# Kernel optimization log

Hardware: AMD Instinct MI355X
Metric: run time of the kernel (lower is better)

Reference implementation:

```python
import jax, jax.numpy as jnp
import numpy as np
import math

H = 16
D_MODEL = 1024
D_K = D_MODEL // H
B, S = 4, 2048
NEG = -1.0e9


def setup_inputs() -> dict:
    key = jax.random.key(0)
    ks = jax.random.split(key, 13)
    scale = 1.0 / math.sqrt(D_MODEL)
    inp = {
        "query": jax.random.normal(ks[0], (B, S, D_MODEL), jnp.float32),
        "key": jax.random.normal(ks[1], (B, S, D_MODEL), jnp.float32),
        "value": jax.random.normal(ks[2], (B, S, D_MODEL), jnp.float32),
        "mask": jax.random.randint(ks[3], (B, S), 0, 2, jnp.int32),
        "Wq": jax.random.normal(ks[4], (D_MODEL, D_MODEL), jnp.float32) * scale,
        "bq": jax.random.normal(ks[5], (D_MODEL,), jnp.float32) * scale,
        "Wk": jax.random.normal(ks[6], (D_MODEL, D_MODEL), jnp.float32) * scale,
        "bk": jax.random.normal(ks[7], (D_MODEL,), jnp.float32) * scale,
        "Wv": jax.random.normal(ks[8], (D_MODEL, D_MODEL), jnp.float32) * scale,
        "bv": jax.random.normal(ks[9], (D_MODEL,), jnp.float32) * scale,
        "Wo": jax.random.normal(ks[10], (D_MODEL, D_MODEL), jnp.float32) * scale,
        "bo": jax.random.normal(ks[11], (D_MODEL,), jnp.float32) * scale,
    }
    return inp


def _split_heads(x):
    # [B, S, D] -> [B, H, S, D_K]
    b, s, _ = x.shape
    return x.reshape(b, s, H, D_K).transpose(0, 2, 1, 3)


def reference(query, key, value, mask, Wq, bq, Wk, bk, Wv, bv, Wo, bo):
    # torch nn.Linear: y = x @ W.T + b
    q = _split_heads(query @ Wq.T + bq)
    k = _split_heads(key @ Wk.T + bk)
    v = _split_heads(value @ Wv.T + bv)
    scores = jnp.einsum("bhqd,bhkd->bhqk", q, k) / math.sqrt(D_K)
    # [B, S] key-padding mask -> broadcast as [B, 1, 1, S] (== torch's [B,1,S,S] repeat)
    m = mask[:, None, None, :]
    scores = jnp.where(m == 0, NEG, scores)
    p = jax.nn.softmax(scores, axis=-1)
    out = jnp.einsum("bhqk,bhkd->bhqd", p, v)  # [B, H, S, D_K]
    out = out.transpose(0, 2, 1, 3).reshape(query.shape[0], -1, D_MODEL)
    return out @ Wo.T + bo
```

## Files before the change

kernel.cpp:

```cpp
#include <hip/hip_runtime.h>


#define DMODEL 1024
#define SLEN 2048
#define NHEAD 16
#define LOG2E 1.44269504088896340736f

typedef __attribute__((ext_vector_type(4))) float f32x4;
typedef __attribute__((ext_vector_type(8))) short bf16x8;
typedef __attribute__((ext_vector_type(4))) int i32x4;
typedef __attribute__((ext_vector_type(2))) int i32x2;

__device__ __forceinline__ unsigned short f2bf(float f) {
  __bf16 h = (__bf16)f;
  union { __bf16 h; unsigned short u; } cv; cv.h = h; return cv.u;
}
__device__ __forceinline__ unsigned pk(float a, float b) {
  return (unsigned)f2bf(a) | ((unsigned)f2bf(b) << 16);
}
__device__ __forceinline__ float fexp2(float x) {
  float r;
  asm("v_exp_f32 %0, %1" : "=v"(r) : "v"(x));
  return r;
}
__device__ __forceinline__ f32x4 zero4() {
  f32x4 z; z[0] = 0.f; z[1] = 0.f; z[2] = 0.f; z[3] = 0.f; return z;
}
__device__ __forceinline__ void gload16(const void* g, void* l) {
  __builtin_amdgcn_global_load_lds(
      (const __attribute__((address_space(1))) unsigned int*)(uintptr_t)g,
      (__attribute__((address_space(3))) unsigned int*)(uintptr_t)l, 16, 0, 0);
}
__device__ __forceinline__ void barrier_lgkm() {
  asm volatile("s_waitcnt lgkmcnt(0)" ::: "memory");
  __builtin_amdgcn_s_barrier();
  __builtin_amdgcn_sched_barrier(0);
}

__global__ __launch_bounds__(256)
void gemm_qkv(const float* __restrict__ xq, const float* __restrict__ xk,
              const float* __restrict__ xv,
              const float* __restrict__ Wq, const float* __restrict__ bq,
              const float* __restrict__ Wk, const float* __restrict__ bk,
              const float* __restrict__ Wv, const float* __restrict__ bv,
              unsigned short* __restrict__ qw, unsigned short* __restrict__ kw,
              unsigned short* __restrict__ vw)
{
  const int bid = blockIdx.x;
  const int wg = (bid & 7) * 192 + (bid >> 3);
  const int z = wg >> 9;
  const int r = wg & 511;
  const int m0 = (r >> 3) * 128;
  const int n0 = (r & 7) * 128;

  const float* __restrict__ X    = (z == 0) ? xq : (z == 1) ? xk : xv;
  const float* __restrict__ W    = (z == 0) ? Wq : (z == 1) ? Wk : Wv;
  const float* __restrict__ bias = (z == 0) ? bq : (z == 1) ? bk : bv;
  const float scale = (z == 0) ? 0.125f * LOG2E : 1.0f;

  const int tid = threadIdx.x;
  const int lane = tid & 63, wid = tid >> 6;
  const int l15 = lane & 15, g = lane >> 4;
  const int wr = wid >> 1, wc = wid & 1;

  __shared__ __align__(16) char LDS[32768];
  unsigned short* TT = (unsigned short*)LDS;

  const int srow = tid >> 1, sh = tid & 1;
  const float* __restrict__ Ag = X + (size_t)(m0 + srow) * DMODEL + sh * 16;
  const float* __restrict__ Bg = W + (size_t)(n0 + srow) * DMODEL + sh * 16;
  const unsigned sw0 = (unsigned)(srow * 64) + (((unsigned)(sh * 2))     ^ ((unsigned)((srow >> 1) & 3))) * 16;
  const unsigned sw1 = (unsigned)(srow * 64) + (((unsigned)(sh * 2 + 1)) ^ ((unsigned)((srow >> 1) & 3))) * 16;

  f32x4 ar4[4], br4[4];
  auto loadA = [&](int kt2) {
    const float* p = Ag + kt2 * 32;
#pragma unroll
    for (int j = 0; j < 4; ++j) ar4[j] = *(const f32x4*)(p + j * 4);
  };
  auto loadB = [&](int kt2) {
    const float* p = Bg + kt2 * 32;
#pragma unroll
    for (int j = 0; j < 4; ++j) br4[j] = *(const f32x4*)(p + j * 4);
  };
  auto packA = [&](int bufsel) {
    char* Ab = LDS + bufsel * 8192;
    i32x4 wv0, wv1;
    wv0[0] = (int)pk(ar4[0][0], ar4[0][1]); wv0[1] = (int)pk(ar4[0][2], ar4[0][3]);
    wv0[2] = (int)pk(ar4[1][0], ar4[1][1]); wv0[3] = (int)pk(ar4[1][2], ar4[1][3]);
    wv1[0] = (int)pk(ar4[2][0], ar4[2][1]); wv1[1] = (int)pk(ar4[2][2], ar4[2][3]);
    wv1[2] = (int)pk(ar4[3][0], ar4[3][1]); wv1[3] = (int)pk(ar4[3][2], ar4[3][3]);
    *(i32x4*)(Ab + sw0) = wv0;
    *(i32x4*)(Ab + sw1) = wv1;
  };
  auto packB = [&](int bufsel) {
    char* Bb = LDS + 16384 + bufsel * 8192;
    i32x4 wv0, wv1;
    wv0[0] = (int)pk(br4[0][0], br4[0][1]); wv0[1] = (int)pk(br4[0][2], br4[0][3]);
    wv0[2] = (int)pk(br4[1][0], br4[1][1]); wv0[3] = (int)pk(br4[1][2], br4[1][3]);
    wv1[0] = (int)pk(br4[2][0], br4[2][1]); wv1[1] = (int)pk(br4[2][2], br4[2][3]);
    wv1[2] = (int)pk(br4[3][0], br4[3][1]); wv1[3] = (int)pk(br4[3][2], br4[3][3]);
    *(i32x4*)(Bb + sw0) = wv0;
    *(i32x4*)(Bb + sw1) = wv1;
  };

  f32x4 acc[4][4];
#pragma unroll
  for (int i = 0; i < 4; ++i)
#pragma unroll
    for (int j = 0; j < 4; ++j) acc[i][j] = zero4();

  loadA(0); loadB(0);
  packA(0); packB(0);
  loadA(1); loadB(1);
  __syncthreads();

  for (int kt = 0; kt < 32; ++kt) {
    const int cur = kt & 1;
    if (kt + 1 < 32) {
      packA(cur ^ 1);
      packB(cur ^ 1);
    }
    if (kt + 2 < 32) {
      loadA(kt + 2);
      loadB(kt + 2);
    }

    const char* Ab = LDS + cur * 8192;
    const char* Bb = LDS + 16384 + cur * 8192;
    bf16x8 afr[4], bfr[4];
#pragma unroll
    for (int i = 0; i < 4; ++i) {
      const int ra = wr * 64 + i * 16 + l15;
      afr[i] = *(const bf16x8*)(Ab + ra * 64 + ((g ^ ((ra >> 1) & 3)) * 16));
      const int rb = wc * 64 + i * 16 + l15;
      bfr[i] = *(const bf16x8*)(Bb + rb * 64 + ((g ^ ((rb >> 1) & 3)) * 16));
    }
#pragma unroll
    for (int mi = 0; mi < 4; ++mi)
#pragma unroll
      for (int ni = 0; ni < 4; ++ni)
        acc[mi][ni] = __builtin_amdgcn_mfma_f32_16x16x32_bf16(
            afr[mi], bfr[ni], acc[mi][ni], 0, 0, 0);

    if (kt + 1 < 32) barrier_lgkm();
  }

  float bv4[4];
#pragma unroll
  for (int ni = 0; ni < 4; ++ni) bv4[ni] = bias[n0 + wc * 64 + ni * 16 + l15];

  if (z == 2) {
    const int bb = m0 >> 11, s0 = m0 & 2047;
#pragma unroll
    for (int p = 0; p < 2; ++p) {
      __syncthreads();
      if (wc == p) {
#pragma unroll
        for (int mi = 0; mi < 4; ++mi)
#pragma unroll
          for (int ni = 0; ni < 4; ++ni)
#pragma unroll
            for (int rr2 = 0; rr2 < 4; ++rr2)
              TT[(ni * 16 + l15) * 136 + wr * 64 + mi * 16 + 4 * g + rr2] =
                  f2bf(acc[mi][ni][rr2] + bv4[ni]);
      }
      __syncthreads();
      const int rr = tid >> 2, cc = (tid & 3) * 32;
      unsigned short* dp = vw + ((size_t)(bb * 1024 + n0 + p * 64 + rr)) * 2048 + s0 + cc;
      const unsigned short* sp = &TT[rr * 136 + cc];
#pragma unroll
      for (int j = 0; j < 4; ++j)
        *(i32x4*)(void*)(dp + j * 8) = *(const i32x4*)(const void*)(sp + j * 8);
    }
    return;
  }

  unsigned short* __restrict__ dst = (z == 0) ? qw : kw;
#pragma unroll
  for (int mi = 0; mi < 4; ++mi) {
#pragma unroll
    for (int ni = 0; ni < 4; ++ni) {
      const int n = n0 + wc * 64 + ni * 16 + l15;
      const int h = n >> 6, d = n & 63;
#pragma unroll
      for (int rr2 = 0; rr2 < 4; ++rr2) {
        const int m = m0 + wr * 64 + mi * 16 + 4 * g + rr2;
        const int b = m >> 11, s = m & 2047;
        const float val = (acc[mi][ni][rr2] + bv4[ni]) * scale;
        dst[((size_t)(b * NHEAD + h) * SLEN + s) * 64 + d] = f2bf(val);
      }
    }
  }
}

__global__ __launch_bounds__(256, 3)
void attn(const unsigned short* __restrict__ q_ws,
          const unsigned short* __restrict__ k_ws,
          const unsigned short* __restrict__ vT,
              const int* __restrict__ mask,
          unsigned short* __restrict__ o_ws)
{
  const int bh = blockIdx.x;
  const int qt = blockIdx.y;
  const int b = bh >> 4, h = bh & 15;
  const int tid = threadIdx.x, w = tid >> 6, lane = tid & 63;
  const int l15 = lane & 15, g = lane >> 4;

  __shared__ __align__(16) unsigned short Kb[2][64 * 64];
  __shared__ __align__(16) unsigned short Vb[2][64 * 64];
  __shared__ __align__(16) unsigned short Pl[4][16 * 64];
  __shared__ __align__(16) float maskf[2048];

  {
    const int4* mp = (const int4*)(mask + b * SLEN);
    const int4 ma = mp[tid * 2], mb = mp[tid * 2 + 1];
    float4 f0, f1;
    f0.x = ma.x ? 0.f : -1e9f; f0.y = ma.y ? 0.f : -1e9f;
    f0.z = ma.z ? 0.f : -1e9f; f0.w = ma.w ? 0.f : -1e9f;
    f1.x = mb.x ? 0.f : -1e9f; f1.y = mb.y ? 0.f : -1e9f;
    f1.z = mb.z ? 0.f : -1e9f; f1.w = mb.w ? 0.f : -1e9f;
    *(float4*)&maskf[tid * 8]     = f0;
    *(float4*)&maskf[tid * 8 + 4] = f1;
  }

  const size_t head = (size_t)bh * SLEN;
  const int r8 = lane >> 3, c8 = lane & 7;
  const int swz = ((c8 ^ r8) * 16);
  const unsigned pswz = (unsigned)((l15 & 7) << 4);

  const int qbase = qt * 128 + w * 32;
  bf16x8 qf[2][2];
  {
    const unsigned short* qp0 = q_ws + (head + qbase + l15) * 64;
    const unsigned short* qp1 = q_ws + (head + qbase + 16 + l15) * 64;
    qf[0][0] = *(const bf16x8*)(qp0 + g * 8);
    qf[0][1] = *(const bf16x8*)(qp0 + 32 + g * 8);
    qf[1][0] = *(const bf16x8*)(qp1 + g * 8);
    qf[1][1] = *(const bf16x8*)(qp1 + 32 + g * 8);
  }

  auto stage = [&](int kt2, int bufi) {
#pragma unroll
    for (int cl = 0; cl < 2; ++cl) {
      const int rr = w * 16 + cl * 8 + r8;
      const char* gk = (const char*)(k_ws + (head + kt2 * 64 + rr) * 64) + swz;
      gload16(gk, &Kb[bufi][(w * 16 + cl * 8) * 64]);
      const char* gv = (const char*)(vT + ((size_t)(bh * 64 + rr)) * SLEN + kt2 * 64) + swz;
      gload16(gv, &Vb[bufi][(w * 16 + cl * 8) * 64]);
    }
  };

  stage(0, 0);
  __syncthreads();

  float m_run[2] = {-1e30f, -1e30f};
  float l_run[2] = {0.f, 0.f};
  f32x4 of[2][4];
#pragma unroll
  for (int qi = 0; qi < 2; ++qi)
#pragma unroll
    for (int n = 0; n < 4; ++n) of[qi][n] = zero4();

  unsigned short* Pw = (unsigned short*)Pl[w];
  int cur = 0;

  for (int kt = 0; kt < 32; ++kt) {
    if (kt + 1 < 32) stage(kt + 1, cur ^ 1);
    const char* Kc = (const char*)Kb[cur];
    const char* Vc = (const char*)Vb[cur];
    const int kv0 = kt * 64;

    f32x4 mv[4];
#pragma unroll
    for (int s = 0; s < 4; ++s) mv[s] = *(const f32x4*)&maskf[kv0 + s * 16 + g * 4];

#pragma unroll
    for (int qi = 0; qi < 2; ++qi) {
      f32x4 sac[4];
#pragma unroll
      for (int s = 0; s < 4; ++s) {
        const char* kr = Kc + (s * 16 + l15) * 128;
        const bf16x8 kf0 = *(const bf16x8*)(kr + ((unsigned)(g * 16) ^ pswz));
        const bf16x8 kf1 = *(const bf16x8*)(kr + ((unsigned)(64 + g * 16) ^ pswz));
        f32x4 zt = mv[s];
        zt = __builtin_amdgcn_mfma_f32_16x16x32_bf16(kf0, qf[qi][0], zt, 0, 0, 0);
        sac[s] = __builtin_amdgcn_mfma_f32_16x16x32_bf16(kf1, qf[qi][1], zt, 0, 0, 0);
      }

      float tmax = -3.0e38f;
#pragma unroll
      for (int s = 0; s < 4; ++s)
#pragma unroll
        for (int rr = 0; rr < 4; ++rr) tmax = fmaxf(tmax, sac[s][rr]);
      tmax = fmaxf(tmax, __shfl_xor(tmax, 16));
      tmax = fmaxf(tmax, __shfl_xor(tmax, 32));
      if (!__all(tmax <= m_run[qi] + 8.f)) {
        const float mnew = fmaxf(m_run[qi], tmax);
        const float alpha = fexp2(m_run[qi] - mnew);
        float af[4];
#pragma unroll
        for (int rr = 0; rr < 4; ++rr) af[rr] = __shfl(alpha, g * 4 + rr);
#pragma unroll
        for (int n = 0; n < 4; ++n)
#pragma unroll
          for (int rr = 0; rr < 4; ++rr) of[qi][n][rr] *= af[rr];
        l_run[qi] *= alpha;
        m_run[qi] = mnew;
      }
      float psum = 0.f;
      unsigned pr[4][2];
#pragma unroll
      for (int s = 0; s < 4; ++s) {
        const float p0 = fexp2(sac[s][0] - m_run[qi]);
        const float p1 = fexp2(sac[s][1] - m_run[qi]);
        const float p2 = fexp2(sac[s][2] - m_run[qi]);
        const float p3 = fexp2(sac[s][3] - m_run[qi]);
        psum += (p0 + p1) + (p2 + p3);
        pr[s][0] = pk(p0, p1); pr[s][1] = pk(p2, p3);
      }
      l_run[qi] += psum;
#pragma unroll
      for (int s = 0; s < 4; ++s) {
        i32x2 wv; wv[0] = (int)pr[s][0]; wv[1] = (int)pr[s][1];
        *(i32x2*)(void*)((char*)Pw + l15 * 128 + ((unsigned)(s * 32 + g * 8) ^ pswz)) = wv;
      }

#pragma unroll
      for (int k2 = 0; k2 < 2; ++k2) {
        const bf16x8 pa = *(const bf16x8*)(const void*)(
            (const char*)Pw + l15 * 128 + ((unsigned)(k2 * 64 + g * 16) ^ pswz));
#pragma unroll
        for (int n = 0; n < 4; ++n) {
          const bf16x8 vf = *(const bf16x8*)(
              Vc + (n * 16 + l15) * 128 + ((unsigned)(k2 * 64 + g * 16) ^ pswz));
          of[qi][n] = __builtin_amdgcn_mfma_f32_16x16x32_bf16(pa, vf, of[qi][n], 0, 0, 0);
        }
      }
    }
    __syncthreads();
    cur ^= 1;
  }

#pragma unroll
  for (int qi = 0; qi < 2; ++qi) {
    float lt = l_run[qi];
    lt += __shfl_xor(lt, 16);
    lt += __shfl_xor(lt, 32);
    float inv[4];
#pragma unroll
    for (int rr = 0; rr < 4; ++rr) inv[rr] = 1.f / __shfl(lt, g * 4 + rr);
    const int qrow0 = qt * 128 + w * 32 + qi * 16;
#pragma unroll
    for (int n = 0; n < 4; ++n) {
      const int d = h * 64 + n * 16 + l15;
#pragma unroll
      for (int rr = 0; rr < 4; ++rr) {
        const int sr = qrow0 + 4 * g + rr;
        o_ws[((size_t)b * SLEN + sr) * DMODEL + d] = f2bf(of[qi][n][rr] * inv[rr]);
      }
    }
  }
}

__global__ __launch_bounds__(256)
void gemm_out(const unsigned short* __restrict__ ow,
              const float* __restrict__ Wo, const float* __restrict__ bo,
              float* __restrict__ out)
{
  const int bid = blockIdx.x;
  const int wg = (bid & 7) * 64 + (bid >> 3);
  const int m0 = (wg >> 3) * 128;
  const int n0 = (wg & 7) * 128;

  const int tid = threadIdx.x;
  const int lane = tid & 63, wid = tid >> 6;
  const int l15 = lane & 15, g = lane >> 4;
  const int wr = wid >> 1, wc = wid & 1;

  __shared__ __align__(16) char LDS[32768];

  const int srow = tid >> 1, sh = tid & 1;
  const unsigned short* __restrict__ Ag = ow + (size_t)(m0 + srow) * DMODEL + sh * 16;
  const float* __restrict__ Bg = Wo + (size_t)(n0 + srow) * DMODEL + sh * 16;
  const unsigned sw0 = (unsigned)(srow * 64) + (((unsigned)(sh * 2))     ^ ((unsigned)((srow >> 1) & 3))) * 16;
  const unsigned sw1 = (unsigned)(srow * 64) + (((unsigned)(sh * 2 + 1)) ^ ((unsigned)((srow >> 1) & 3))) * 16;

  i32x4 ar2[2];
  f32x4 br4[4];
  auto loadA = [&](int kt2) {
    const unsigned short* p = Ag + kt2 * 32;
    ar2[0] = *(const i32x4*)(p);
    ar2[1] = *(const i32x4*)(p + 8);
  };
  auto loadB = [&](int kt2) {
    const float* p = Bg + kt2 * 32;
#pragma unroll
    for (int j = 0; j < 4; ++j) br4[j] = *(const f32x4*)(p + j * 4);
  };
  auto packA = [&](int bufsel) {
    char* Ab = LDS + bufsel * 8192;
    *(i32x4*)(Ab + sw0) = ar2[0];
    *(i32x4*)(Ab + sw1) = ar2[1];
  };
  auto packB = [&](int bufsel) {
    char* Bb = LDS + 16384 + bufsel * 8192;
    i32x4 wv0, wv1;
    wv0[0] = (int)pk(br4[0][0], br4[0][1]); wv0[1] = (int)pk(br4[0][2], br4[0][3]);
    wv0[2] = (int)pk(br4[1][0], br4[1][1]); wv0[3] = (int)pk(br4[1][2], br4[1][3]);
    wv1[0] = (int)pk(br4[2][0], br4[2][1]); wv1[1] = (int)pk(br4[2][2], br4[2][3]);
    wv1[2] = (int)pk(br4[3][0], br4[3][1]); wv1[3] = (int)pk(br4[3][2], br4[3][3]);
    *(i32x4*)(Bb + sw0) = wv0;
    *(i32x4*)(Bb + sw1) = wv1;
  };

  f32x4 acc[4][4];
#pragma unroll
  for (int i = 0; i < 4; ++i)
#pragma unroll
    for (int j = 0; j < 4; ++j) acc[i][j] = zero4();

  loadA(0); loadB(0);
  packA(0); packB(0);
  loadA(1); loadB(1);
  __syncthreads();

  for (int kt = 0; kt < 32; ++kt) {
    const int cur = kt & 1;
    if (kt + 1 < 32) {
      packA(cur ^ 1);
      packB(cur ^ 1);
    }
    if (kt + 2 < 32) {
      loadA(kt + 2);
      loadB(kt + 2);
    }

    const char* Ab = LDS + cur * 8192;
    const char* Bb = LDS + 16384 + cur * 8192;
    bf16x8 afr[4], bfr[4];
#pragma unroll
    for (int i = 0; i < 4; ++i) {
      const int ra = wr * 64 + i * 16 + l15;
      afr[i] = *(const bf16x8*)(Ab + ra * 64 + ((g ^ ((ra >> 1) & 3)) * 16));
      const int rb = wc * 64 + i * 16 + l15;
      bfr[i] = *(const bf16x8*)(Bb + rb * 64 + ((g ^ ((rb >> 1) & 3)) * 16));
    }
#pragma unroll
    for (int mi = 0; mi < 4; ++mi)
#pragma unroll
      for (int ni = 0; ni < 4; ++ni)
        acc[mi][ni] = __builtin_amdgcn_mfma_f32_16x16x32_bf16(
            afr[mi], bfr[ni], acc[mi][ni], 0, 0, 0);

    if (kt + 1 < 32) barrier_lgkm();
  }

  float bv4[4];
#pragma unroll
  for (int ni = 0; ni < 4; ++ni) bv4[ni] = bo[n0 + wc * 64 + ni * 16 + l15];
#pragma unroll
  for (int mi = 0; mi < 4; ++mi) {
#pragma unroll
    for (int ni = 0; ni < 4; ++ni) {
      const int n = n0 + wc * 64 + ni * 16 + l15;
#pragma unroll
      for (int rr = 0; rr < 4; ++rr) {
        const int m = m0 + wr * 64 + mi * 16 + 4 * g + rr;
        out[(size_t)m * DMODEL + n] = acc[mi][ni][rr] + bv4[ni];
      }
    }
  }
}

extern "C" void kernel_launch(void* const* d_in, const int* in_sizes, int n_in,
                              void* d_out, int out_size, void* d_ws, size_t ws_size,
                              hipStream_t stream) {
  const float* query = (const float*)d_in[0];
  const float* key_  = (const float*)d_in[1];
  const float* value = (const float*)d_in[2];
  const int*   mask  = (const int*)d_in[3];
  const float* Wq = (const float*)d_in[4];
  const float* bq = (const float*)d_in[5];
  const float* Wk = (const float*)d_in[6];
  const float* bk = (const float*)d_in[7];
  const float* Wv = (const float*)d_in[8];
  const float* bv = (const float*)d_in[9];
  const float* Wo = (const float*)d_in[10];
  const float* bo = (const float*)d_in[11];
  float* out = (float*)d_out;

  char* ws = (char*)d_ws;
  unsigned short* q_ws = (unsigned short*)(ws);
  unsigned short* k_ws = (unsigned short*)(ws + (size_t)16777216);
  unsigned short* vT   = (unsigned short*)(ws + (size_t)2 * 16777216);
  unsigned short* o_ws = (unsigned short*)(ws + (size_t)3 * 16777216);

  gemm_qkv<<<dim3(1536), 256, 0, stream>>>(query, key_, value,
                                           Wq, bq, Wk, bk, Wv, bv,
                                           q_ws, k_ws, vT);
  attn<<<dim3(64, 16), 256, 0, stream>>>(q_ws, k_ws, vT, mask, o_ws);
  gemm_out<<<dim3(512), 256, 0, stream>>>(o_ws, Wo, bo, out);
}
```

Measured before the change: 267.7 us.

## Pre-convert inputs and weights to bf16 and stream GEMM tiles via direct-to-LDS loads

Adds a conversion kernel that casts the fp32 activations and weights to bf16 in workspace. The QKV and output GEMMs then load tiles with global_load_lds DMA instead of fp32 register loads plus in-kernel packing. When the workspace is too small, only the weights are converted and A keeps the old path. The aim is to halve the bytes each GEMM reads and drop VALU packing from the main loop, at the cost of an extra pass over the inputs. The DMA path drops the LDS swizzle, which risks bank conflicts.

```diff
diff --git a/kernel.cpp b/kernel.cpp
--- a/kernel.cpp
+++ b/kernel.cpp
@@ -31,20 +31,57 @@
       (const __attribute__((address_space(1))) unsigned int*)(uintptr_t)g,
       (__attribute__((address_space(3))) unsigned int*)(uintptr_t)l, 16, 0, 0);
 }
-__device__ __forceinline__ void barrier_lgkm() {
-  asm volatile("s_waitcnt lgkmcnt(0)" ::: "memory");
-  __builtin_amdgcn_s_barrier();
-  __builtin_amdgcn_sched_barrier(0);
-}
 
 __global__ __launch_bounds__(256)
-void gemm_qkv(const float* __restrict__ xq, const float* __restrict__ xk,
-              const float* __restrict__ xv,
-              const float* __restrict__ Wq, const float* __restrict__ bq,
-              const float* __restrict__ Wk, const float* __restrict__ bk,
-              const float* __restrict__ Wv, const float* __restrict__ bv,
-              unsigned short* __restrict__ qw, unsigned short* __restrict__ kw,
-              unsigned short* __restrict__ vw)
+void cvt_pre(const float* __restrict__ xq, const float* __restrict__ xk,
+             const float* __restrict__ xv,
+             const float* __restrict__ Wq, const float* __restrict__ Wk,
+             const float* __restrict__ Wv, const float* __restrict__ Wo,
+             unsigned short* __restrict__ xbf, unsigned short* __restrict__ wbf,
+             int full)
+{
+  const long nchunk = full ? 3670016L : 393216L;
+  const long stride = (long)gridDim.x * blockDim.x;
+  for (long c = (long)blockIdx.x * blockDim.x + threadIdx.x; c < nchunk; c += stride) {
+    const float* src; unsigned short* dst; long off;
+    if (full) {
+      if (c < 3145728L) {
+        const int i = (int)(c >> 20);
+        off = (c & 1048575L) * 8;
+        src = (i == 0) ? xq : (i == 1) ? xk : xv;
+        dst = xbf + (size_t)i * 8388608;
+      } else {
+        const long d = c - 3145728L;
+        const int j = (int)(d >> 17);
+        off = (d & 131071L) * 8;
+        src = (j == 0) ? Wq : (j == 1) ? Wk : (j == 2) ? Wv : Wo;
+        dst = wbf + (size_t)j * 1048576;
+      }
+    } else {
+      const int j = (int)(c >> 17);
+      off = (c & 131071L) * 8;
+      src = (j == 0) ? Wq : (j == 1) ? Wk : Wv;
+      dst = wbf + (size_t)j * 1048576;
+    }
+    const float4 a = *(const float4*)(src + off);
+    const float4 b = *(const float4*)(src + off + 4);
+    i32x4 o;
+    o[0] = (int)pk(a.x, a.y); o[1] = (int)pk(a.z, a.w);
+    o[2] = (int)pk(b.x, b.y); o[3] = (int)pk(b.z, b.w);
+    *(i32x4*)(dst + off) = o;
+  }
+}
+
+template <bool ADMA>
+__global__ __launch_bounds__(256)
+void gemm_qkv_t(const float* __restrict__ xq, const float* __restrict__ xk,
+                const float* __restrict__ xv,
+                const unsigned short* __restrict__ xbf,
+                const unsigned short* __restrict__ wbf,
+                const float* __restrict__ bq, const float* __restrict__ bk,
+                const float* __restrict__ bv,
+                unsigned short* __restrict__ qw, unsigned short* __restrict__ kw,
+                unsigned short* __restrict__ vw)
 {
   const int bid = blockIdx.x;
   const int wg = (bid & 7) * 192 + (bid >> 3);
@@ -53,8 +90,9 @@
   const int m0 = (r >> 3) * 128;
   const int n0 = (r & 7) * 128;
 
-  const float* __restrict__ X    = (z == 0) ? xq : (z == 1) ? xk : xv;
-  const float* __restrict__ W    = (z == 0) ? Wq : (z == 1) ? Wk : Wv;
+  const float* __restrict__ X = (z == 0) ? xq : (z == 1) ? xk : xv;
+  const unsigned short* __restrict__ Xb = xbf + (size_t)z * 8388608;
+  const unsigned short* __restrict__ Wb = wbf + (size_t)z * 1048576;
   const float* __restrict__ bias = (z == 0) ? bq : (z == 1) ? bk : bv;
   const float scale = (z == 0) ? 0.125f * LOG2E : 1.0f;
 
@@ -66,22 +104,36 @@
   __shared__ __align__(16) char LDS[32768];
   unsigned short* TT = (unsigned short*)LDS;
 
+  auto dmaB = [&](int kt2, int bufsel) {
+    char* dst = LDS + 16384 + bufsel * 8192;
+#pragma unroll
+    for (int q = 0; q < 2; ++q) {
+      const int r0 = wid * 32 + q * 16;
+      const unsigned short* src = Wb + (size_t)(n0 + r0 + (lane >> 2)) * 1024
+                                     + kt2 * 32 + (lane & 3) * 8;
+      gload16(src, dst + r0 * 64);
+    }
+  };
+  auto dmaA = [&](int kt2, int bufsel) {
+    char* dst = LDS + bufsel * 8192;
+#pragma unroll
+    for (int q = 0; q < 2; ++q) {
+      const int r0 = wid * 32 + q * 16;
+      const unsigned short* src = Xb + (size_t)(m0 + r0 + (lane >> 2)) * 1024
+                                     + kt2 * 32 + (lane & 3) * 8;
+      gload16(src, dst + r0 * 64);
+    }
+  };
+
   const int srow = tid >> 1, sh = tid & 1;
   const float* __restrict__ Ag = X + (size_t)(m0 + srow) * DMODEL + sh * 16;
-  const float* __restrict__ Bg = W + (size_t)(n0 + srow) * DMODEL + sh * 16;
   const unsigned sw0 = (unsigned)(srow * 64) + (((unsigned)(sh * 2))     ^ ((unsigned)((srow >> 1) & 3))) * 16;
   const unsigned sw1 = (unsigned)(srow * 64) + (((unsigned)(sh * 2 + 1)) ^ ((unsigned)((srow >> 1) & 3))) * 16;
-
-  f32x4 ar4[4], br4[4];
+  f32x4 ar4[4];
   auto loadA = [&](int kt2) {
     const float* p = Ag + kt2 * 32;
 #pragma unroll
     for (int j = 0; j < 4; ++j) ar4[j] = *(const f32x4*)(p + j * 4);
-  };
-  auto loadB = [&](int kt2) {
-    const float* p = Bg + kt2 * 32;
-#pragma unroll
-    for (int j = 0; j < 4; ++j) br4[j] = *(const f32x4*)(p + j * 4);
   };
   auto packA = [&](int bufsel) {
     char* Ab = LDS + bufsel * 8192;
@@ -93,16 +145,6 @@
     *(i32x4*)(Ab + sw0) = wv0;
     *(i32x4*)(Ab + sw1) = wv1;
   };
-  auto packB = [&](int bufsel) {
-    char* Bb = LDS + 16384 + bufsel * 8192;
-    i32x4 wv0, wv1;
-    wv0[0] = (int)pk(br4[0][0], br4[0][1]); wv0[1] = (int)pk(br4[0][2], br4[0][3]);
-    wv0[2] = (int)pk(br4[1][0], br4[1][1]); wv0[3] = (int)pk(br4[1][2], br4[1][3]);
-    wv1[0] = (int)pk(br4[2][0], br4[2][1]); wv1[1] = (int)pk(br4[2][2], br4[2][3]);
-    wv1[2] = (int)pk(br4[3][0], br4[3][1]); wv1[3] = (int)pk(br4[3][2], br4[3][3]);
-    *(i32x4*)(Bb + sw0) = wv0;
-    *(i32x4*)(Bb + sw1) = wv1;
-  };
 
   f32x4 acc[4][4];
 #pragma unroll
@@ -110,21 +152,22 @@
 #pragma unroll
     for (int j = 0; j < 4; ++j) acc[i][j] = zero4();
 
-  loadA(0); loadB(0);
-  packA(0); packB(0);
-  loadA(1); loadB(1);
+  if (ADMA) {
+    dmaA(0, 0);
+  } else {
+    loadA(0); packA(0); loadA(1);
+  }
+  dmaB(0, 0);
   __syncthreads();
 
   for (int kt = 0; kt < 32; ++kt) {
     const int cur = kt & 1;
     if (kt + 1 < 32) {
-      packA(cur ^ 1);
-      packB(cur ^ 1);
-    }
-    if (kt + 2 < 32) {
-      loadA(kt + 2);
-      loadB(kt + 2);
-    }
+      dmaB(kt + 1, cur ^ 1);
+      if (ADMA) dmaA(kt + 1, cur ^ 1);
+      else      packA(cur ^ 1);
+    }
+    if (!ADMA && kt + 2 < 32) loadA(kt + 2);
 
     const char* Ab = LDS + cur * 8192;
     const char* Bb = LDS + 16384 + cur * 8192;
@@ -132,9 +175,11 @@
 #pragma unroll
     for (int i = 0; i < 4; ++i) {
       const int ra = wr * 64 + i * 16 + l15;
-      afr[i] = *(const bf16x8*)(Ab + ra * 64 + ((g ^ ((ra >> 1) & 3)) * 16));
+      const unsigned ab = ADMA ? (unsigned)(g * 16)
+                               : ((unsigned)(g ^ ((ra >> 1) & 3)) * 16);
+      afr[i] = *(const bf16x8*)(Ab + ra * 64 + ab);
       const int rb = wc * 64 + i * 16 + l15;
-      bfr[i] = *(const bf16x8*)(Bb + rb * 64 + ((g ^ ((rb >> 1) & 3)) * 16));
+      bfr[i] = *(const bf16x8*)(Bb + rb * 64 + g * 16);
     }
 #pragma unroll
     for (int mi = 0; mi < 4; ++mi)
@@ -143,7 +188,7 @@
         acc[mi][ni] = __builtin_amdgcn_mfma_f32_16x16x32_bf16(
             afr[mi], bfr[ni], acc[mi][ni], 0, 0, 0);
 
-    if (kt + 1 < 32) barrier_lgkm();
+    if (kt + 1 < 32) __syncthreads();
   }
 
   float bv4[4];
@@ -198,7 +243,7 @@
 void attn(const unsigned short* __restrict__ q_ws,
           const unsigned short* __restrict__ k_ws,
           const unsigned short* __restrict__ vT,
-              const int* __restrict__ mask,
+          const int* __restrict__ mask,
           unsigned short* __restrict__ o_ws)
 {
   const int bh = blockIdx.x;
@@ -363,10 +408,12 @@
   }
 }
 
+template <bool DMA>
 __global__ __launch_bounds__(256)
-void gemm_out(const unsigned short* __restrict__ ow,
-              const float* __restrict__ Wo, const float* __restrict__ bo,
-              float* __restrict__ out)
+void gemm_out_t(const unsigned short* __restrict__ ow,
+                const unsigned short* __restrict__ wob,
+                const float* __restrict__ Wo, const float* __restrict__ bo,
+                float* __restrict__ out)
 {
   const int bid = blockIdx.x;
   const int wg = (bid & 7) * 64 + (bid >> 3);
@@ -380,12 +427,32 @@
 
   __shared__ __align__(16) char LDS[32768];
 
+  auto dmaA = [&](int kt2, int bufsel) {
+    char* dst = LDS + bufsel * 8192;
+#pragma unroll
+    for (int q = 0; q < 2; ++q) {
+      const int r0 = wid * 32 + q * 16;
+      const unsigned short* src = ow + (size_t)(m0 + r0 + (lane >> 2)) * 1024
+                                     + kt2 * 32 + (lane & 3) * 8;
+      gload16(src, dst + r0 * 64);
+    }
+  };
+  auto dmaB = [&](int kt2, int bufsel) {
+    char* dst = LDS + 16384 + bufsel * 8192;
+#pragma unroll
+    for (int q = 0; q < 2; ++q) {
+      const int r0 = wid * 32 + q * 16;
+      const unsigned short* src = wob + (size_t)(n0 + r0 + (lane >> 2)) * 1024
+                                      + kt2 * 32 + (lane & 3) * 8;
+      gload16(src, dst + r0 * 64);
+    }
+  };
+
   const int srow = tid >> 1, sh = tid & 1;
   const unsigned short* __restrict__ Ag = ow + (size_t)(m0 + srow) * DMODEL + sh * 16;
   const float* __restrict__ Bg = Wo + (size_t)(n0 + srow) * DMODEL + sh * 16;
   const unsigned sw0 = (unsigned)(srow * 64) + (((unsigned)(sh * 2))     ^ ((unsigned)((srow >> 1) & 3))) * 16;
   const unsigned sw1 = (unsigned)(srow * 64) + (((unsigned)(sh * 2 + 1)) ^ ((unsigned)((srow >> 1) & 3))) * 16;
-
   i32x4 ar2[2];
   f32x4 br4[4];
   auto loadA = [&](int kt2) {
@@ -420,21 +487,22 @@
 #pragma unroll
     for (int j = 0; j < 4; ++j) acc[i][j] = zero4();
 
-  loadA(0); loadB(0);
-  packA(0); packB(0);
-  loadA(1); loadB(1);
+  if (DMA) {
+    dmaA(0, 0); dmaB(0, 0);
+  } else {
+    loadA(0); loadB(0);
+    packA(0); packB(0);
+    loadA(1); loadB(1);
+  }
   __syncthreads();
 
   for (int kt = 0; kt < 32; ++kt) {
     const int cur = kt & 1;
     if (kt + 1 < 32) {
-      packA(cur ^ 1);
-      packB(cur ^ 1);
-    }
-    if (kt + 2 < 32) {
-      loadA(kt + 2);
-      loadB(kt + 2);
-    }
+      if (DMA) { dmaA(kt + 1, cur ^ 1); dmaB(kt + 1, cur ^ 1); }
+      else     { packA(cur ^ 1); packB(cur ^ 1); }
+    }
+    if (!DMA && kt + 2 < 32) { loadA(kt + 2); loadB(kt + 2); }
 
     const char* Ab = LDS + cur * 8192;
     const char* Bb = LDS + 16384 + cur * 8192;
@@ -442,9 +510,13 @@
 #pragma unroll
     for (int i = 0; i < 4; ++i) {
       const int ra = wr * 64 + i * 16 + l15;
-      afr[i] = *(const bf16x8*)(Ab + ra * 64 + ((g ^ ((ra >> 1) & 3)) * 16));
+      const unsigned ab = DMA ? (unsigned)(g * 16)
+                              : ((unsigned)(g ^ ((ra >> 1) & 3)) * 16);
+      afr[i] = *(const bf16x8*)(Ab + ra * 64 + ab);
       const int rb = wc * 64 + i * 16 + l15;
-      bfr[i] = *(const bf16x8*)(Bb + rb * 64 + ((g ^ ((rb >> 1) & 3)) * 16));
+      const unsigned bb2 = DMA ? (unsigned)(g * 16)
+                               : ((unsigned)(g ^ ((rb >> 1) & 3)) * 16);
+      bfr[i] = *(const bf16x8*)(Bb + rb * 64 + bb2);
     }
 #pragma unroll
     for (int mi = 0; mi < 4; ++mi)
@@ -453,7 +525,7 @@
         acc[mi][ni] = __builtin_amdgcn_mfma_f32_16x16x32_bf16(
             afr[mi], bfr[ni], acc[mi][ni], 0, 0, 0);
 
-    if (kt + 1 < 32) barrier_lgkm();
+    if (kt + 1 < 32) __syncthreads();
   }
 
   float bv4[4];
@@ -490,15 +562,31 @@
   const float* bo = (const float*)d_in[11];
   float* out = (float*)d_out;
 
+  const size_t MiB = 1048576;
   char* ws = (char*)d_ws;
   unsigned short* q_ws = (unsigned short*)(ws);
-  unsigned short* k_ws = (unsigned short*)(ws + (size_t)16777216);
-  unsigned short* vT   = (unsigned short*)(ws + (size_t)2 * 16777216);
-  unsigned short* o_ws = (unsigned short*)(ws + (size_t)3 * 16777216);
-
-  gemm_qkv<<<dim3(1536), 256, 0, stream>>>(query, key_, value,
-                                           Wq, bq, Wk, bk, Wv, bv,
-                                           q_ws, k_ws, vT);
+  unsigned short* k_ws = (unsigned short*)(ws + 16 * MiB);
+  unsigned short* vT   = (unsigned short*)(ws + 32 * MiB);
+  unsigned short* o_ws = (unsigned short*)(ws + 48 * MiB);
+
+  const bool big = ws_size >= 120 * MiB;
+  unsigned short* xbf = big ? (unsigned short*)(ws + 64 * MiB) : (unsigned short*)0;
+  unsigned short* wbf = big ? (unsigned short*)(ws + 112 * MiB)
+                            : (unsigned short*)(ws + 48 * MiB);
+
+  cvt_pre<<<dim3(2048), 256, 0, stream>>>(query, key_, value, Wq, Wk, Wv, Wo,
+                                          xbf, wbf, big ? 1 : 0);
+  if (big)
+    gemm_qkv_t<true><<<dim3(1536), 256, 0, stream>>>(query, key_, value, xbf, wbf,
+                                                     bq, bk, bv, q_ws, k_ws, vT);
+  else
+    gemm_qkv_t<false><<<dim3(1536), 256, 0, stream>>>(query, key_, value, xbf, wbf,
+                                                      bq, bk, bv, q_ws, k_ws, vT);
   attn<<<dim3(64, 16), 256, 0, stream>>>(q_ws, k_ws, vT, mask, o_ws);
-  gemm_out<<<dim3(512), 256, 0, stream>>>(o_ws, Wo, bo, out);
-}
+  if (big)
+    gemm_out_t<true><<<dim3(512), 256, 0, stream>>>(o_ws, wbf + (size_t)3 * 1048576,
+                                                    Wo, bo, out);
+  else
+    gemm_out_t<false><<<dim3(512), 256, 0, stream>>>(o_ws, (const unsigned short*)0,
+                                                     Wo, bo, out);
+}
```

Result: no change. 268.0 us (+0.1%).
